# Kernel optimization log

Measured on AMD Instinct MI355X. Metric: run time of the kernel, lower is better.

## Reference

```python
import jax, jax.numpy as jnp
import numpy as np

N_NODES = 100000
N_EDGES = 1600000
IN_DIM = 256
HEADS = 4
OUT_DIM = 32
ALPHA = 0.2  # leaky relu slope


def setup_inputs() -> dict:
    key = jax.random.key(0)
    k1, k2, k3, k4, k5, k6 = jax.random.split(key, 6)
    feature = jax.random.normal(k1, (N_NODES, IN_DIM), dtype=jnp.float32)
    src = jax.random.randint(k2, (N_EDGES,), 0, N_NODES, dtype=jnp.int32)
    dst = jax.random.randint(k3, (N_EDGES,), 0, N_NODES, dtype=jnp.int32)
    W_fc = jax.random.normal(k4, (IN_DIM, HEADS * OUT_DIM), dtype=jnp.float32) * 0.05
    attn_l = jax.random.normal(k5, (1, HEADS, OUT_DIM), dtype=jnp.float32) * 0.1
    attn_r = jax.random.normal(k6, (1, HEADS, OUT_DIM), dtype=jnp.float32) * 0.1
    return {"feature": feature, "src": src, "dst": dst, "W_fc": W_fc,
            "attn_l": attn_l, "attn_r": attn_r}


def reference(feature, src, dst, W_fc, attn_l, attn_r):
    # node projection: [N, H, D]
    ft = (feature @ W_fc).reshape(feature.shape[0], HEADS, OUT_DIM)
    # per-node attention scores: [N, H]
    a1 = jnp.sum(ft * attn_l, axis=-1)
    a2 = jnp.sum(ft * attn_r, axis=-1)
    # edge attention logits: gather src/dst + leaky relu -> [E, H]
    e = a1[src] + a2[dst]
    e = jnp.where(e > 0, e, ALPHA * e)
    # segment softmax over destination groups
    n = feature.shape[0]
    e_max = jax.ops.segment_max(e, dst, num_segments=n)  # [N, H]
    e_exp = jnp.exp(e - e_max[dst])
    e_sum = jax.ops.segment_sum(e_exp, dst, num_segments=n)  # [N, H]
    alpha = e_exp / e_sum[dst]  # [E, H]
    # weighted scatter-sum aggregation: [N, H, D]
    msgs = ft[src] * alpha[:, :, None]
    out = jax.ops.segment_sum(msgs, dst, num_segments=n)
    return out
```

## Files before the change

### kernel.cpp

```cpp
#include <hip/hip_runtime.h>
#include <hip/hip_fp16.h>

#define N_NODES 100000
#define N_EDGES 1600000
#define IN_DIM 256
#define HEADS 4
#define OUT_DIM 32
#define NHD 128
#define LEAKY 0.2f
#define INV_LN2 1.4426950408889634f

#define SS_CAP (N_EDGES + 4 * N_NODES)

#define SCAN_BLOCK 1024
#define N_SCAN_BLOCKS ((N_NODES + SCAN_BLOCK - 1) / SCAN_BLOCK)

typedef _Float16 f16x8 __attribute__((ext_vector_type(8)));
typedef _Float16 f16x4 __attribute__((ext_vector_type(4)));
typedef float    f32x4 __attribute__((ext_vector_type(4)));

__global__ void init_kernel(int* __restrict__ deg, int* __restrict__ src_sorted,
                            float* __restrict__ a1, __half* __restrict__ ft) {
    int i = blockIdx.x * blockDim.x + threadIdx.x;
    if (i < N_NODES) deg[i] = 0;
    if (i < SS_CAP) src_sorted[i] = N_NODES;
    if (i < HEADS) a1[N_NODES * HEADS + i] = -1e30f;
    if (i < 64) ((unsigned*)(ft + (size_t)N_NODES * NHD))[i] = 0u;
}

__global__ void wprep_kernel(const float* __restrict__ W,
                             _Float16* __restrict__ Wt_hi,
                             _Float16* __restrict__ Wt_lo) {
    int i = blockIdx.x * blockDim.x + threadIdx.x;
    if (i < NHD * IN_DIM) {
        int c = i >> 8;
        int k = i & 255;
        float w = W[(size_t)k * NHD + c];
        _Float16 hi = (_Float16)w;
        _Float16 lo = (_Float16)(w - (float)hi);
        Wt_hi[i] = hi;
        Wt_lo[i] = lo;
    }
}

__launch_bounds__(256, 4)
__global__ void gemm_kernel(const float* __restrict__ feature,
                            const _Float16* __restrict__ Wt_hi,
                            const _Float16* __restrict__ Wt_lo,
                            const float* __restrict__ attn_l,
                            const float* __restrict__ attn_r,
                            __half* __restrict__ ft,
                            float* __restrict__ a1,
                            float* __restrict__ a2) {
    __shared__ _Float16 sA [128][40];
    __shared__ _Float16 sWh[128][40];
    __shared__ _Float16 sWl[128][40];

    const int t    = threadIdx.x;
    const int w    = t >> 6;
    const int lane = t & 63;
    const int l15  = lane & 15;
    const int kg   = lane >> 4;
    const int nb   = blockIdx.x * 128;

    f32x4 acc[8][2];
#pragma unroll
    for (int nt = 0; nt < 8; ++nt) {
        acc[nt][0] = (f32x4){0.f, 0.f, 0.f, 0.f};
        acc[nt][1] = (f32x4){0.f, 0.f, 0.f, 0.f};
    }

    for (int kt = 0; kt < 8; ++kt) {
        __syncthreads();
#pragma unroll
        for (int p = 0; p < 4; ++p) {
            int idx  = t + p * 256;
            int node = idx >> 3;
            int c4   = idx & 7;
            float4 v = make_float4(0.f, 0.f, 0.f, 0.f);
            if (nb + node < N_NODES)
                v = *(const float4*)&feature[(size_t)(nb + node) * IN_DIM + kt * 32 + c4 * 4];
            f16x4 hh;
            hh[0] = (_Float16)v.x; hh[1] = (_Float16)v.y;
            hh[2] = (_Float16)v.z; hh[3] = (_Float16)v.w;
            *(f16x4*)&sA[node][c4 * 4] = hh;
        }
#pragma unroll
        for (int p = 0; p < 2; ++p) {
            int c   = t + p * 256;
            int col = c >> 2;
            int kc  = c & 3;
            *(f16x8*)&sWh[col][kc * 8] =
                *(const f16x8*)&Wt_hi[(size_t)col * IN_DIM + kt * 32 + kc * 8];
            *(f16x8*)&sWl[col][kc * 8] =
                *(const f16x8*)&Wt_lo[(size_t)col * IN_DIM + kt * 32 + kc * 8];
        }
        __syncthreads();

        f16x8 wh0 = *(const f16x8*)&sWh[w * 32 + l15][kg * 8];
        f16x8 wh1 = *(const f16x8*)&sWh[w * 32 + 16 + l15][kg * 8];
        f16x8 wl0 = *(const f16x8*)&sWl[w * 32 + l15][kg * 8];
        f16x8 wl1 = *(const f16x8*)&sWl[w * 32 + 16 + l15][kg * 8];

#pragma unroll
        for (int nt = 0; nt < 8; ++nt) {
            f16x8 af = *(const f16x8*)&sA[nt * 16 + l15][kg * 8];
            acc[nt][0] = __builtin_amdgcn_mfma_f32_16x16x32_f16(wh0, af, acc[nt][0], 0, 0, 0);
            acc[nt][0] = __builtin_amdgcn_mfma_f32_16x16x32_f16(wl0, af, acc[nt][0], 0, 0, 0);
            acc[nt][1] = __builtin_amdgcn_mfma_f32_16x16x32_f16(wh1, af, acc[nt][1], 0, 0, 0);
            acc[nt][1] = __builtin_amdgcn_mfma_f32_16x16x32_f16(wl1, af, acc[nt][1], 0, 0, 0);
        }
    }

    float al8[8], ar8[8];
#pragma unroll
    for (int ct = 0; ct < 2; ++ct)
#pragma unroll
        for (int r = 0; r < 4; ++r) {
            int cb = ct * 16 + kg * 4 + r;
            al8[ct * 4 + r] = attn_l[w * 32 + cb];
            ar8[ct * 4 + r] = attn_r[w * 32 + cb];
        }

#pragma unroll
    for (int nt = 0; nt < 8; ++nt) {
        int node = nb + nt * 16 + l15;
        bool valid = node < N_NODES;
        if (valid) {
            f16x4 s0, s1;
#pragma unroll
            for (int r = 0; r < 4; ++r) {
                s0[r] = (_Float16)acc[nt][0][r];
                s1[r] = (_Float16)acc[nt][1][r];
            }
            *(f16x4*)&ft[(size_t)node * NHD + w * 32 + kg * 4]      = s0;
            *(f16x4*)&ft[(size_t)node * NHD + w * 32 + 16 + kg * 4] = s1;
        }
        float pl = 0.f, pr = 0.f;
#pragma unroll
        for (int ct = 0; ct < 2; ++ct)
#pragma unroll
            for (int r = 0; r < 4; ++r) {
                pl = fmaf(acc[nt][ct][r], al8[ct * 4 + r], pl);
                pr = fmaf(acc[nt][ct][r], ar8[ct * 4 + r], pr);
            }
        pl += __shfl_xor(pl, 16); pl += __shfl_xor(pl, 32);
        pr += __shfl_xor(pr, 16); pr += __shfl_xor(pr, 32);
        if (kg == 0 && valid) {
            a1[node * HEADS + w] = pl * INV_LN2;
            a2[node * HEADS + w] = pr * INV_LN2;
        }
    }
}

__global__ void hist_kernel(const int* __restrict__ dst, int* __restrict__ deg,
                            int* __restrict__ edge_pos) {
    int i = blockIdx.x * blockDim.x + threadIdx.x;
    if (i < N_EDGES) edge_pos[i] = atomicAdd(&deg[dst[i]], 1);
}

__global__ void scan1_kernel(const int* __restrict__ deg,
                             int* __restrict__ partial,
                             int* __restrict__ blocksum) {
    __shared__ int wsum[16];
    const int tid  = threadIdx.x;
    const int lane = tid & 63;
    const int wid  = tid >> 6;
    const int i    = blockIdx.x * SCAN_BLOCK + tid;
    int v = (i < N_NODES) ? ((deg[i] + 3) & ~3) : 0;
    int x = v;
#pragma unroll
    for (int o = 1; o < 64; o <<= 1) {
        int y = __shfl_up(x, o);
        if (lane >= o) x += y;
    }
    if (lane == 63) wsum[wid] = x;
    __syncthreads();
    if (wid == 0 && lane < 16) {
        int w = wsum[lane];
#pragma unroll
        for (int o = 1; o < 16; o <<= 1) {
            int y = __shfl_up(w, o);
            if (lane >= o) w += y;
        }
        wsum[lane] = w;
    }
    __syncthreads();
    int woff = (wid > 0) ? wsum[wid - 1] : 0;
    if (i < N_NODES) partial[i] = woff + x - v;
    if (tid == SCAN_BLOCK - 1) blocksum[blockIdx.x] = wsum[15];
}

__global__ void scan2_kernel(const int* __restrict__ blocksum,
                             int* __restrict__ blockoff,
                             int* __restrict__ offsets) {
    __shared__ int wtot[2];
    const int tid  = threadIdx.x;
    const int lane = tid & 63;
    const int wid  = tid >> 6;
    int v = (tid < N_SCAN_BLOCKS) ? blocksum[tid] : 0;
    int x = v;
#pragma unroll
    for (int o = 1; o < 64; o <<= 1) {
        int y = __shfl_up(x, o);
        if (lane >= o) x += y;
    }
    if (lane == 63) wtot[wid] = x;
    __syncthreads();
    int add = (wid == 1) ? wtot[0] : 0;
    if (tid < N_SCAN_BLOCKS) blockoff[tid] = add + x - v;
    if (tid == N_SCAN_BLOCKS - 1) offsets[N_NODES] = add + x;
}

__global__ void scan3_kernel(const int* __restrict__ partial,
                             const int* __restrict__ blockoff,
                             int* __restrict__ offsets) {
    int i = blockIdx.x * SCAN_BLOCK + threadIdx.x;
    if (i < N_NODES) offsets[i] = partial[i] + blockoff[blockIdx.x];
}

__global__ void fill_kernel(const int* __restrict__ src, const int* __restrict__ dst,
                            const int* __restrict__ offsets,
                            const int* __restrict__ edge_pos,
                            int* __restrict__ src_sorted) {
    int i = blockIdx.x * blockDim.x + threadIdx.x;
    if (i < N_EDGES) {
        int idx = offsets[dst[i]] + edge_pos[i];
        src_sorted[idx] = src[i];
    }
}

__launch_bounds__(256)
__global__ void agg_kernel(const __half* __restrict__ ft,
                           const float* __restrict__ a1,
                           const float* __restrict__ a2,
                           const int* __restrict__ offsets,
                           const int* __restrict__ src_sorted,
                           float* __restrict__ out) {
    const int wave = threadIdx.x >> 6;
    const int lane = threadIdx.x & 63;
    const int node = blockIdx.x * 4 + wave;
    if (node >= N_NODES) return;
    const int h = lane >> 4;
    const int lane2 = lane * 2;

    const float a2v = a2[node * HEADS + h];
    const int e0 = offsets[node];
    const int e1 = offsets[node + 1];

    float accx = 0.f, accy = 0.f, wsum = 0.f;

    for (int e = e0; e < e1; e += 4) {
        int4 s4 = *(const int4*)&src_sorted[e];
        float b0 = a1[s4.x * HEADS + h];
        float b1 = a1[s4.y * HEADS + h];
        float b2 = a1[s4.z * HEADS + h];
        float b3 = a1[s4.w * HEADS + h];
        __half2 h0 = *(const __half2*)&ft[s4.x * NHD + lane2];
        __half2 h1 = *(const __half2*)&ft[s4.y * NHD + lane2];
        __half2 h2 = *(const __half2*)&ft[s4.z * NHD + lane2];
        __half2 h3 = *(const __half2*)&ft[s4.w * NHD + lane2];
        float t0 = b0 + a2v, t1 = b1 + a2v, t2 = b2 + a2v, t3 = b3 + a2v;
        float w0 = exp2f(fmaxf(t0, LEAKY * t0));
        float w1 = exp2f(fmaxf(t1, LEAKY * t1));
        float w2 = exp2f(fmaxf(t2, LEAKY * t2));
        float w3 = exp2f(fmaxf(t3, LEAKY * t3));
        float2 v0 = __half22float2(h0);
        float2 v1 = __half22float2(h1);
        float2 v2 = __half22float2(h2);
        float2 v3 = __half22float2(h3);
        accx = fmaf(w0, v0.x, accx); accy = fmaf(w0, v0.y, accy);
        accx = fmaf(w1, v1.x, accx); accy = fmaf(w1, v1.y, accy);
        accx = fmaf(w2, v2.x, accx); accy = fmaf(w2, v2.y, accy);
        accx = fmaf(w3, v3.x, accx); accy = fmaf(w3, v3.y, accy);
        wsum += (w0 + w1) + (w2 + w3);
    }
    float inv = (e1 > e0) ? 1.f / wsum : 0.f;
    float2 o = make_float2(accx * inv, accy * inv);
    *(float2*)&out[(size_t)node * NHD + lane2] = o;
}

extern "C" void kernel_launch(void* const* d_in, const int* in_sizes, int n_in,
                              void* d_out, int out_size, void* d_ws, size_t ws_size,
                              hipStream_t stream) {
    const float* feature = (const float*)d_in[0];
    const int*   src     = (const int*)d_in[1];
    const int*   dst     = (const int*)d_in[2];
    const float* W       = (const float*)d_in[3];
    const float* attn_l  = (const float*)d_in[4];
    const float* attn_r  = (const float*)d_in[5];
    float*       out     = (float*)d_out;

    char* ws = (char*)d_ws;
    size_t off = 0;
    auto alloc = [&](size_t bytes) -> void* {
        void* p = ws + off;
        off = (off + bytes + 255) & ~(size_t)255;
        return p;
    };
    __half*    ft        = (__half*)alloc((size_t)(N_NODES + 1) * NHD * 2);
    float*     a1        = (float*)alloc((size_t)(N_NODES + 1) * HEADS * 4);
    float*     a2        = (float*)alloc((size_t)N_NODES * HEADS * 4);
    int*       deg       = (int*)alloc((size_t)N_NODES * 4);
    int*       offsets   = (int*)alloc((size_t)(N_NODES + 1) * 4);
    int*       src_sorted= (int*)alloc((size_t)SS_CAP * 4);
    int*       edge_pos  = (int*)alloc((size_t)N_EDGES * 4);
    int*       partial   = (int*)alloc((size_t)N_NODES * 4);
    int*       blocksum  = (int*)alloc((size_t)N_SCAN_BLOCKS * 4);
    int*       blockoff  = (int*)alloc((size_t)N_SCAN_BLOCKS * 4);
    _Float16*  Wt_hi     = (_Float16*)alloc((size_t)NHD * IN_DIM * 2);
    _Float16*  Wt_lo     = (_Float16*)alloc((size_t)NHD * IN_DIM * 2);

    init_kernel<<<(SS_CAP + 255) / 256, 256, 0, stream>>>(deg, src_sorted, a1, ft);
    wprep_kernel<<<(NHD * IN_DIM + 255) / 256, 256, 0, stream>>>(W, Wt_hi, Wt_lo);
    gemm_kernel<<<(N_NODES + 127) / 128, 256, 0, stream>>>(feature, Wt_hi, Wt_lo,
                                                           attn_l, attn_r, ft, a1, a2);
    hist_kernel<<<(N_EDGES + 255) / 256, 256, 0, stream>>>(dst, deg, edge_pos);
    scan1_kernel<<<N_SCAN_BLOCKS, SCAN_BLOCK, 0, stream>>>(deg, partial, blocksum);
    scan2_kernel<<<1, 128, 0, stream>>>(blocksum, blockoff, offsets);
    scan3_kernel<<<N_SCAN_BLOCKS, SCAN_BLOCK, 0, stream>>>(partial, blockoff, offsets);
    fill_kernel<<<(N_EDGES + 255) / 256, 256, 0, stream>>>(src, dst, offsets, edge_pos, src_sorted);
    agg_kernel<<<(N_NODES + 3) / 4, 256, 0, stream>>>(ft, a1, a2, offsets, src_sorted, out);
}
```

Before: 396.9 us.

## Split wave into four edge groups with 16-byte feature loads; pad-fill only gaps

The aggregation kernel now has each quarter-wave handle a different edge. Each lane loads 8 fp16 features with one 16-byte load and keeps 8 accumulators, then the quarter-waves are combined with cross-lane shuffles. This replaces four 4-byte gathers per lane per step with wider, more coalesced loads, but adds a reduction and leaves three quarters of the lanes idle at store time. Separately, the full sentinel initialisation of src_sorted is replaced by a small kernel that writes sentinels only into each node's padding slots. This cuts about 2M stores at the cost of one extra launch and a serial per-thread loop.

Measured after the change: 392.0 us. About the same (-1.2%).

```diff
diff --git a/kernel.cpp b/kernel.cpp
--- a/kernel.cpp
+++ b/kernel.cpp
@@ -19,11 +19,10 @@
 typedef _Float16 f16x4 __attribute__((ext_vector_type(4)));
 typedef float    f32x4 __attribute__((ext_vector_type(4)));
 
-__global__ void init_kernel(int* __restrict__ deg, int* __restrict__ src_sorted,
-                            float* __restrict__ a1, __half* __restrict__ ft) {
+__global__ void init_kernel(int* __restrict__ deg, float* __restrict__ a1,
+                            __half* __restrict__ ft) {
     int i = blockIdx.x * blockDim.x + threadIdx.x;
     if (i < N_NODES) deg[i] = 0;
-    if (i < SS_CAP) src_sorted[i] = N_NODES;
     if (i < HEADS) a1[N_NODES * HEADS + i] = -1e30f;
     if (i < 64) ((unsigned*)(ft + (size_t)N_NODES * NHD))[i] = 0u;
 }
@@ -219,6 +218,17 @@
     if (i < N_NODES) offsets[i] = partial[i] + blockoff[blockIdx.x];
 }
 
+__global__ void padfill_kernel(const int* __restrict__ deg,
+                               const int* __restrict__ offsets,
+                               int* __restrict__ src_sorted) {
+    int i = blockIdx.x * blockDim.x + threadIdx.x;
+    if (i < N_NODES) {
+        int base = offsets[i] + deg[i];
+        int end  = offsets[i + 1];
+        for (int k = base; k < end; ++k) src_sorted[k] = N_NODES;
+    }
+}
+
 __global__ void fill_kernel(const int* __restrict__ src, const int* __restrict__ dst,
                             const int* __restrict__ offsets,
                             const int* __restrict__ edge_pos,
@@ -241,43 +251,45 @@
     const int lane = threadIdx.x & 63;
     const int node = blockIdx.x * 4 + wave;
     if (node >= N_NODES) return;
-    const int h = lane >> 4;
-    const int lane2 = lane * 2;
+    const int q     = lane >> 4;
+    const int li    = lane & 15;
+    const int h     = li >> 2;
+    const int dbase = li * 8;
 
     const float a2v = a2[node * HEADS + h];
     const int e0 = offsets[node];
     const int e1 = offsets[node + 1];
 
-    float accx = 0.f, accy = 0.f, wsum = 0.f;
+    float acc[8] = {0.f, 0.f, 0.f, 0.f, 0.f, 0.f, 0.f, 0.f};
+    float wsum = 0.f;
 
     for (int e = e0; e < e1; e += 4) {
-        int4 s4 = *(const int4*)&src_sorted[e];
-        float b0 = a1[s4.x * HEADS + h];
-        float b1 = a1[s4.y * HEADS + h];
-        float b2 = a1[s4.z * HEADS + h];
-        float b3 = a1[s4.w * HEADS + h];
-        __half2 h0 = *(const __half2*)&ft[s4.x * NHD + lane2];
-        __half2 h1 = *(const __half2*)&ft[s4.y * NHD + lane2];
-        __half2 h2 = *(const __half2*)&ft[s4.z * NHD + lane2];
-        __half2 h3 = *(const __half2*)&ft[s4.w * NHD + lane2];
-        float t0 = b0 + a2v, t1 = b1 + a2v, t2 = b2 + a2v, t3 = b3 + a2v;
-        float w0 = exp2f(fmaxf(t0, LEAKY * t0));
-        float w1 = exp2f(fmaxf(t1, LEAKY * t1));
-        float w2 = exp2f(fmaxf(t2, LEAKY * t2));
-        float w3 = exp2f(fmaxf(t3, LEAKY * t3));
-        float2 v0 = __half22float2(h0);
-        float2 v1 = __half22float2(h1);
-        float2 v2 = __half22float2(h2);
-        float2 v3 = __half22float2(h3);
-        accx = fmaf(w0, v0.x, accx); accy = fmaf(w0, v0.y, accy);
-        accx = fmaf(w1, v1.x, accx); accy = fmaf(w1, v1.y, accy);
-        accx = fmaf(w2, v2.x, accx); accy = fmaf(w2, v2.y, accy);
-        accx = fmaf(w3, v3.x, accx); accy = fmaf(w3, v3.y, accy);
-        wsum += (w0 + w1) + (w2 + w3);
-    }
+        int s    = src_sorted[e + q];
+        float b  = a1[s * HEADS + h];
+        float t  = b + a2v;
+        float w  = exp2f(fmaxf(t, LEAKY * t));
+        f16x8 v  = *(const f16x8*)&ft[s * NHD + dbase];
+#pragma unroll
+        for (int i = 0; i < 8; ++i)
+            acc[i] = fmaf(w, (float)v[i], acc[i]);
+        wsum += w;
+    }
+
+#pragma unroll
+    for (int i = 0; i < 8; ++i) {
+        acc[i] += __shfl_xor(acc[i], 16);
+        acc[i] += __shfl_xor(acc[i], 32);
+    }
+    wsum += __shfl_xor(wsum, 16);
+    wsum += __shfl_xor(wsum, 32);
+
     float inv = (e1 > e0) ? 1.f / wsum : 0.f;
-    float2 o = make_float2(accx * inv, accy * inv);
-    *(float2*)&out[(size_t)node * NHD + lane2] = o;
+    if (q == 0) {
+        float4 o0 = make_float4(acc[0] * inv, acc[1] * inv, acc[2] * inv, acc[3] * inv);
+        float4 o1 = make_float4(acc[4] * inv, acc[5] * inv, acc[6] * inv, acc[7] * inv);
+        *(float4*)&out[(size_t)node * NHD + dbase]     = o0;
+        *(float4*)&out[(size_t)node * NHD + dbase + 4] = o1;
+    }
 }
 
 extern "C" void kernel_launch(void* const* d_in, const int* in_sizes, int n_in,
@@ -311,7 +323,7 @@
     _Float16*  Wt_hi     = (_Float16*)alloc((size_t)NHD * IN_DIM * 2);
     _Float16*  Wt_lo     = (_Float16*)alloc((size_t)NHD * IN_DIM * 2);
 
-    init_kernel<<<(SS_CAP + 255) / 256, 256, 0, stream>>>(deg, src_sorted, a1, ft);
+    init_kernel<<<(N_NODES + 255) / 256, 256, 0, stream>>>(deg, a1, ft);
     wprep_kernel<<<(NHD * IN_DIM + 255) / 256, 256, 0, stream>>>(W, Wt_hi, Wt_lo);
     gemm_kernel<<<(N_NODES + 127) / 128, 256, 0, stream>>>(feature, Wt_hi, Wt_lo,
                                                            attn_l, attn_r, ft, a1, a2);
@@ -319,6 +331,7 @@
     scan1_kernel<<<N_SCAN_BLOCKS, SCAN_BLOCK, 0, stream>>>(deg, partial, blocksum);
     scan2_kernel<<<1, 128, 0, stream>>>(blocksum, blockoff, offsets);
     scan3_kernel<<<N_SCAN_BLOCKS, SCAN_BLOCK, 0, stream>>>(partial, blockoff, offsets);
+    padfill_kernel<<<(N_NODES + 255) / 256, 256, 0, stream>>>(deg, offsets, src_sorted);
     fill_kernel<<<(N_EDGES + 255) / 256, 256, 0, stream>>>(src, dst, offsets, edge_pos, src_sorted);
     agg_kernel<<<(N_NODES + 3) / 4, 256, 0, stream>>>(ft, a1, a2, offsets, src_sorted, out);
 }
```
